# Performance work log

Hardware: AMD Instinct MI355X
Metric: run time of the kernel (lower is better)

The kernel has to match this reference:

```python
import jax, jax.numpy as jnp
import numpy as np

B, NL, C, H, W = 4, 2048, 128, 128, 128
N_PTS0, N_PTS1 = 32, 8
SCALE = N_PTS0 // N_PTS1  # MaxPool1d kernel/stride
FEATURE_DIM = 5
BN_EPS = 1e-5


def setup_inputs() -> dict:
    key = jax.random.key(0)
    ks = jax.random.split(key, 12)
    fm = jax.random.normal(ks[0], (B, C, H, W), dtype=jnp.float32)
    lines = jax.random.uniform(ks[1], (B, NL, 2, 2), dtype=jnp.float32) * 128.0
    P = C // 2
    s = 0.05
    return {
        "feature_map": fm,
        "lines": lines,
        # Bottleneck1D params (BatchNorm in eval mode: running_mean=0, running_var=1)
        "bn1_g": jnp.ones((C,), jnp.float32), "bn1_b": jnp.zeros((C,), jnp.float32),
        "conv1_w": jax.random.normal(ks[2], (P, C, 1), jnp.float32) * s,
        "conv1_b": jnp.zeros((P,), jnp.float32),
        "bn2_g": jnp.ones((P,), jnp.float32), "bn2_b": jnp.zeros((P,), jnp.float32),
        "conv2_w": jax.random.normal(ks[3], (P, P, 3), jnp.float32) * s,
        "conv2_b": jnp.zeros((P,), jnp.float32),
        "bn3_g": jnp.ones((P,), jnp.float32), "bn3_b": jnp.zeros((P,), jnp.float32),
        "conv3_w": jax.random.normal(ks[4], (C, P, 1), jnp.float32) * s,
        "conv3_b": jnp.zeros((C,), jnp.float32),
        # fc2: ReLU -> Linear(dim_loi*n_pts1 + 5, 4)
        "fc2_w": jax.random.normal(ks[5], (4, C * N_PTS1 + FEATURE_DIM), jnp.float32) * s,
        "fc2_b": jnp.zeros((4,), jnp.float32),
    }


def _bn(x, g, b):
    # eval-mode BatchNorm1d with running_mean=0, running_var=1
    return x * (g / jnp.sqrt(1.0 + BN_EPS))[None, :, None] + b[None, :, None]


def _conv1d(x, w, b, pad):
    y = jax.lax.conv_general_dilated(x, w, (1,), [(pad, pad)],
                                     dimension_numbers=("NCH", "OIH", "NCH"))
    return y + b[None, :, None]


def _loi_gather(fm, lines):
    # sample points along each line: [B, NL, N_PTS0, 2]
    lam = jnp.linspace(0.0, 1.0, N_PTS0, dtype=jnp.float32)[None, None, :, None]
    p = lines[:, :, 0:1, :] * lam + lines[:, :, 1:2, :] * (1.0 - lam) - 0.5
    p = p.reshape(B, -1, 2)                      # [B, NL*N_PTS0, 2]
    px, py = p[..., 0], p[..., 1]
    px0 = jnp.clip(jnp.floor(px), 0.0, 127.0)
    py0 = jnp.clip(jnp.floor(py), 0.0, 127.0)
    px1 = jnp.clip(px0 + 1.0, 0.0, 127.0)
    py1 = jnp.clip(py0 + 1.0, 0.0, 127.0)
    px0l, py0l = px0.astype(jnp.int32), py0.astype(jnp.int32)
    px1l, py1l = px1.astype(jnp.int32), py1.astype(jnp.int32)

    gather = jax.vmap(lambda f, yi, xi: f[:, yi, xi])  # [C, P] per image
    # weights exactly as in the torch source
    xp = (gather(fm, py0l, px0l) * ((px1 - px) * (py1 - py))[:, None, :]
          + gather(fm, py1l, px0l) * ((px - px0) * (py1 - py))[:, None, :]
          + gather(fm, py0l, px1l) * ((px1 - px) * (py - py0))[:, None, :]
          + gather(fm, py1l, px1l) * ((px - px0) * (py - py0))[:, None, :])
    # [B, C, NL*N_PTS0] -> [B*NL, C, N_PTS0]
    xp = xp.reshape(B, C, NL, N_PTS0).transpose(0, 2, 1, 3).reshape(B * NL, C, N_PTS0)
    return xp


def reference(feature_map, lines, bn1_g, bn1_b, conv1_w, conv1_b,
              bn2_g, bn2_b, conv2_w, conv2_b, bn3_g, bn3_b,
              conv3_w, conv3_b, fc2_w, fc2_b):
    xp = _loi_gather(feature_map, lines)               # [B*NL, C, N_PTS0]
    # MaxPool1d(SCALE, SCALE)
    x = xp.reshape(B * NL, C, N_PTS1, SCALE).max(axis=-1)
    # Bottleneck1D residual block
    y = jax.nn.relu(_bn(x, bn1_g, bn1_b))
    y = _conv1d(y, conv1_w, conv1_b, 0)
    y = jax.nn.relu(_bn(y, bn2_g, bn2_b))
    y = _conv1d(y, conv2_w, conv2_b, 1)
    y = jax.nn.relu(_bn(y, bn3_g, bn3_b))
    y = _conv1d(y, conv3_w, conv3_b, 0)
    x = x + y                                          # [B*NL, C, N_PTS1]
    # line geometry feature (use_cood=1, use_slop=1)
    xyu, xyv = lines[:, :, 0, :], lines[:, :, 1, :]
    u2v = jnp.sqrt(((xyu - xyv) ** 2).sum(-1, keepdims=True)).clip(min=1e-6)
    f = jnp.concatenate([xyu / 128.0, xyv / 128.0, u2v], axis=-1)
    f = f.reshape(B * NL, FEATURE_DIM)
    # concat + fc2 (ReLU -> Linear)
    x = jnp.concatenate([x.reshape(B * NL, C * N_PTS1), f], axis=1)
    logits = jax.nn.relu(x) @ fc2_w.T + fc2_b
    prob = jax.nn.softmax(logits, axis=1)
    return logits, prob
```

## Files before the change

### kernel.cpp

```cpp
#include <hip/hip_runtime.h>
#include <math.h>

#define BB 4
#define NLL 2048
#define CC 128
#define HH 128
#define WW 128
#define NPTS0 32
#define NPTS1 8
#define PP 64
#define FDIM 5
#define FCK (CC*NPTS1 + FDIM)
#define FCKP 1032

typedef __attribute__((ext_vector_type(8))) short bf16x8;
typedef __attribute__((ext_vector_type(4))) float f32x4;

__device__ __forceinline__ unsigned short f2bf(float f) {
    union { float f; unsigned u; } v; v.f = f;
    unsigned u = v.u;
    return (unsigned short)((u + 0x7fffu + ((u >> 16) & 1u)) >> 16);
}
__device__ __forceinline__ float bf2f(unsigned short s) {
    union { unsigned u; float f; } v; v.u = ((unsigned)s) << 16;
    return v.f;
}

__global__ __launch_bounds__(256)
void transpose_prep(const float* __restrict__ fm, const float* __restrict__ w1,
                    const float* __restrict__ w2, const float* __restrict__ w3,
                    const float* __restrict__ fcw,
                    unsigned short* __restrict__ fmT,
                    unsigned short* __restrict__ W1b,
                    unsigned short* __restrict__ W2b,
                    unsigned short* __restrict__ W3b,
                    float* __restrict__ fcwP) {
    const int t = threadIdx.x;
    if (blockIdx.x >= 512) {
        int gid = (blockIdx.x - 512) * 256 + t;
        for (int e = gid; e < 32800; e += 4096) {
            if (e < 8192) {
                W1b[e] = f2bf(w1[e]);
            } else if (e < 20480) {
                int g = e - 8192;
                int tt = g >> 12, r = g & 4095;
                int p = r >> 6, q = r & 63;
                W2b[tt * 4096 + p * 64 + q] = f2bf(w2[p * 192 + q * 3 + tt]);
            } else if (e < 28672) {
                int g = e - 20480;
                W3b[g] = f2bf(w3[g]);
            } else {
                int g = e - 28672;
                int o = g / FCKP, r = g - o * FCKP;
                fcwP[g] = (r < FCK) ? fcw[o * FCK + r] : 0.0f;
            }
        }
        return;
    }
    __shared__ unsigned short tile[2][128 * 72];
    const int by = blockIdx.x;
    const int b = by >> 7, y = by & 127;
    const float* src = fm + ((size_t)b * CC) * (HH * WW) + (size_t)y * WW;
    const int x4 = (t & 31) * 4;
    const int xh = x4 >> 6, xl = x4 & 63;
    #pragma unroll
    for (int i = 0; i < 16; ++i) {
        int r = (t >> 5) + 8 * i;
        float4 v = *(const float4*)&src[(size_t)r * (HH * WW) + x4];
        ushort4 u;
        u.x = f2bf(v.x); u.y = f2bf(v.y); u.z = f2bf(v.z); u.w = f2bf(v.w);
        *(ushort4*)&tile[xh][r * 72 + (xl ^ (r & 28))] = u;
    }
    __syncthreads();
    const int c4 = (t & 31) * 4;
    #pragma unroll
    for (int h = 0; h < 2; ++h) {
        unsigned short* dst = fmT + ((size_t)by * WW + h * 64) * CC;
        #pragma unroll
        for (int i = 0; i < 8; ++i) {
            int x = (t >> 5) + 8 * i;
            ushort4 u;
            u.x = tile[h][(c4 + 0) * 72 + (x ^ ((c4 + 0) & 28))];
            u.y = tile[h][(c4 + 1) * 72 + (x ^ ((c4 + 1) & 28))];
            u.z = tile[h][(c4 + 2) * 72 + (x ^ ((c4 + 2) & 28))];
            u.w = tile[h][(c4 + 3) * 72 + (x ^ ((c4 + 3) & 28))];
            *(ushort4*)&dst[(size_t)x * CC + c4] = u;
        }
    }
}

__global__ __launch_bounds__(256, 8)
void line_mfma(const unsigned short* __restrict__ fmT,
               const float* __restrict__ lines,
               const float* __restrict__ bn1_g, const float* __restrict__ bn1_b,
               const unsigned short* __restrict__ W1b, const float* __restrict__ b1,
               const float* __restrict__ bn2_g, const float* __restrict__ bn2_b,
               const unsigned short* __restrict__ W2b, const float* __restrict__ b2,
               const float* __restrict__ bn3_g, const float* __restrict__ bn3_b,
               const unsigned short* __restrict__ W3b, const float* __restrict__ b3,
               const float* __restrict__ fcwP,  const float* __restrict__ fcb,
               float* __restrict__ out) {
    __shared__ __align__(16) char smem[19200];
    int*   s_oA = (int*)(smem + 0);
    int*   s_oB = (int*)(smem + 512);
    int*   s_oC = (int*)(smem + 1024);
    int*   s_oD = (int*)(smem + 1536);
    float* s_wA = (float*)(smem + 2048);
    float* s_wB = (float*)(smem + 2560);
    float* s_wC = (float*)(smem + 3072);
    float* s_wD = (float*)(smem + 3584);
    unsigned short* s_z1 = (unsigned short*)(smem + 0);
    unsigned short* s_xs = (unsigned short*)(smem + 5760);
    unsigned short* s_z2 = (unsigned short*)(smem + 14464);
    float* s_red = (float*)(smem + 19072);

    const int bx  = blockIdx.x;
    const int L0  = bx * 4;
    const int b   = bx >> 9;
    const int tid = threadIdx.x;
    const int lane = tid & 63;
    const int wv   = tid >> 6;
    const int quad = lane >> 4;
    const int l16  = lane & 15;
    const float inv_s = 1.0f / sqrtf(1.0f + 1e-5f);

    if (tid < 128) {
        int line = tid >> 5, pt = tid & 31;
        const float* ln = lines + (size_t)(L0 + line) * 4;
        float lam = (float)pt * (1.0f / 31.0f);
        float om  = 1.0f - lam;
        float px = ln[0] * lam + ln[2] * om - 0.5f;
        float py = ln[1] * lam + ln[3] * om - 0.5f;
        float px0 = fminf(fmaxf(floorf(px), 0.0f), 127.0f);
        float py0 = fminf(fmaxf(floorf(py), 0.0f), 127.0f);
        float px1 = fminf(px0 + 1.0f, 127.0f);
        float py1 = fminf(py0 + 1.0f, 127.0f);
        int ix0 = (int)px0, ix1 = (int)px1, iy0 = (int)py0, iy1 = (int)py1;
        s_oA[tid] = (iy0 * WW + ix0) * CC;
        s_oB[tid] = (iy1 * WW + ix0) * CC;
        s_oC[tid] = (iy0 * WW + ix1) * CC;
        s_oD[tid] = (iy1 * WW + ix1) * CC;
        float ax = px1 - px, bxv = px - px0, ay = py1 - py, byv = py - py0;
        s_wA[tid] = ax  * ay;
        s_wB[tid] = bxv * ay;
        s_wC[tid] = ax  * byv;
        s_wD[tid] = bxv * byv;
    }
    __syncthreads();

    #pragma unroll 1
    for (int h = 0; h < 2; ++h) {
        int m = h * 16 + (tid >> 4);
        int line = m >> 3, k = m & 7;
        int c8 = (tid & 15) * 8;
        const unsigned short* base = fmT + (size_t)b * (HH * WW * CC) + c8;
        float acc[8];
        #pragma unroll
        for (int i = 0; i < 8; ++i) acc[i] = -INFINITY;
        #pragma unroll
        for (int j = 0; j < 4; ++j) {
            int pt = line * 32 + k * 4 + j;
            bf16x8 rA = *(const bf16x8*)(base + s_oA[pt]);
            bf16x8 rB = *(const bf16x8*)(base + s_oB[pt]);
            bf16x8 rC = *(const bf16x8*)(base + s_oC[pt]);
            bf16x8 rD = *(const bf16x8*)(base + s_oD[pt]);
            float wA = s_wA[pt], wB = s_wB[pt], wC = s_wC[pt], wD = s_wD[pt];
            #pragma unroll
            for (int i = 0; i < 8; ++i) {
                float v = wA * bf2f((unsigned short)rA[i])
                        + wB * bf2f((unsigned short)rB[i])
                        + wC * bf2f((unsigned short)rC[i])
                        + wD * bf2f((unsigned short)rD[i]);
                acc[i] = fmaxf(acc[i], v);
            }
        }
        bf16x8 pk;
        #pragma unroll
        for (int i = 0; i < 8; ++i) pk[i] = (short)f2bf(acc[i]);
        *(bf16x8*)&s_xs[m * 136 + c8] = pk;
    }
    __syncthreads();

    {
        int mh = wv & 1, nh = wv >> 1;
        int mrow = mh * 16 + l16;
        bf16x8 afr[4];
        #pragma unroll
        for (int kc = 0; kc < 4; ++kc) {
            bf16x8 x = *(const bf16x8*)&s_xs[mrow * 136 + kc * 32 + quad * 8];
            int c0 = kc * 32 + quad * 8;
            float4 g0 = *(const float4*)(bn1_g + c0);
            float4 g1 = *(const float4*)(bn1_g + c0 + 4);
            float4 bb0 = *(const float4*)(bn1_b + c0);
            float4 bb1 = *(const float4*)(bn1_b + c0 + 4);
            float gs[8] = {g0.x, g0.y, g0.z, g0.w, g1.x, g1.y, g1.z, g1.w};
            float bs[8] = {bb0.x, bb0.y, bb0.z, bb0.w, bb1.x, bb1.y, bb1.z, bb1.w};
            bf16x8 pk;
            #pragma unroll
            for (int i = 0; i < 8; ++i) {
                float v = fmaxf(bf2f((unsigned short)x[i]) * (gs[i] * inv_s) + bs[i], 0.0f);
                pk[i] = (short)f2bf(v);
            }
            afr[kc] = pk;
        }
        #pragma unroll
        for (int sub = 0; sub < 2; ++sub) {
            int p = nh * 32 + sub * 16 + l16;
            f32x4 acc = {0.f, 0.f, 0.f, 0.f};
            #pragma unroll
            for (int kc = 0; kc < 4; ++kc) {
                bf16x8 bf = *(const bf16x8*)(W1b + p * 128 + kc * 32 + quad * 8);
                acc = __builtin_amdgcn_mfma_f32_16x16x32_bf16(afr[kc], bf, acc, 0, 0, 0);
            }
            float s2 = bn2_g[p] * inv_s, bb2 = bn2_b[p], cb = b1[p];
            #pragma unroll
            for (int r = 0; r < 4; ++r) {
                int mm = mh * 16 + quad * 4 + r;
                int lline = mm >> 3, kk = mm & 7;
                float v = fmaxf((acc[r] + cb) * s2 + bb2, 0.0f);
                s_z1[lline * 720 + (kk + 1) * 72 + p] = f2bf(v);
            }
        }
        #pragma unroll
        for (int e = tid; e < 512; e += 256) {
            int lline = e >> 7;
            int rr = (e >> 6) & 1;
            int q = e & 63;
            s_z1[lline * 720 + (rr ? 9 : 0) * 72 + q] = 0;
        }
    }
    __syncthreads();

    {
        int mh = wv & 1, nh = wv >> 1;
        int mrow = mh * 16 + l16;
        int linea = mrow >> 3, ka = mrow & 7;
        const unsigned short* arow = s_z1 + linea * 720 + ka * 72;
        bf16x8 afr[3][2];
        #pragma unroll
        for (int t = 0; t < 3; ++t)
            #pragma unroll
            for (int kc = 0; kc < 2; ++kc)
                afr[t][kc] = *(const bf16x8*)&arow[t * 72 + kc * 32 + quad * 8];
        #pragma unroll
        for (int sub = 0; sub < 2; ++sub) {
            int p = nh * 32 + sub * 16 + l16;
            f32x4 acc = {0.f, 0.f, 0.f, 0.f};
            #pragma unroll
            for (int t = 0; t < 3; ++t) {
                #pragma unroll
                for (int kc = 0; kc < 2; ++kc) {
                    bf16x8 bf = *(const bf16x8*)(W2b + t * 4096 + p * 64 + kc * 32 + quad * 8);
                    acc = __builtin_amdgcn_mfma_f32_16x16x32_bf16(afr[t][kc], bf, acc, 0, 0, 0);
                }
            }
            float s3 = bn3_g[p] * inv_s, bb3 = bn3_b[p], cb = b2[p];
            #pragma unroll
            for (int r = 0; r < 4; ++r) {
                int mm = mh * 16 + quad * 4 + r;
                float v = fmaxf((acc[r] + cb) * s3 + bb3, 0.0f);
                s_z2[mm * 72 + p] = f2bf(v);
            }
        }
    }
    __syncthreads();

    float p0 = 0.f, p1 = 0.f, p2 = 0.f, p3 = 0.f;
    {
        int mh = wv & 1;
        int n0 = (wv >> 1) * 64;
        int mrow = mh * 16 + l16;
        bf16x8 a0 = *(const bf16x8*)&s_z2[mrow * 72 + quad * 8];
        bf16x8 a1 = *(const bf16x8*)&s_z2[mrow * 72 + 32 + quad * 8];
        int kbase = (quad & 1) * 4;
        #pragma unroll
        for (int sub = 0; sub < 4; ++sub) {
            int c = n0 + sub * 16 + l16;
            f32x4 acc = {0.f, 0.f, 0.f, 0.f};
            bf16x8 bf0 = *(const bf16x8*)(W3b + c * 64 + quad * 8);
            bf16x8 bf1 = *(const bf16x8*)(W3b + c * 64 + 32 + quad * 8);
            acc = __builtin_amdgcn_mfma_f32_16x16x32_bf16(a0, bf0, acc, 0, 0, 0);
            acc = __builtin_amdgcn_mfma_f32_16x16x32_bf16(a1, bf1, acc, 0, 0, 0);
            float cb = b3[c];
            int idx = c * 8 + kbase;
            float4 w0 = *(const float4*)(fcwP + 0 * FCKP + idx);
            float4 w1v = *(const float4*)(fcwP + 1 * FCKP + idx);
            float4 w2v = *(const float4*)(fcwP + 2 * FCKP + idx);
            float4 w3v = *(const float4*)(fcwP + 3 * FCKP + idx);
            const float* w0a = (const float*)&w0;
            const float* w1a = (const float*)&w1v;
            const float* w2a = (const float*)&w2v;
            const float* w3a = (const float*)&w3v;
            #pragma unroll
            for (int r = 0; r < 4; ++r) {
                int mm = mh * 16 + quad * 4 + r;
                float xv = bf2f(s_xs[mm * 136 + c]);
                float v = fmaxf(xv + acc[r] + cb, 0.0f);
                p0 = fmaf(v, w0a[r], p0);
                p1 = fmaf(v, w1a[r], p1);
                p2 = fmaf(v, w2a[r], p2);
                p3 = fmaf(v, w3a[r], p3);
            }
        }
    }
    #pragma unroll
    for (int off = 16; off >= 1; off >>= 1) {
        p0 += __shfl_down(p0, off);
        p1 += __shfl_down(p1, off);
        p2 += __shfl_down(p2, off);
        p3 += __shfl_down(p3, off);
    }
    if ((lane & 31) == 0) {
        int h = lane >> 5;
        s_red[wv * 8 + h * 4 + 0] = p0;
        s_red[wv * 8 + h * 4 + 1] = p1;
        s_red[wv * 8 + h * 4 + 2] = p2;
        s_red[wv * 8 + h * 4 + 3] = p3;
    }
    __syncthreads();

    if (tid < 4) {
        int line = tid;
        int wa = line >> 1;
        int h  = (line & 1) * 4;
        float lg[4];
        #pragma unroll
        for (int o = 0; o < 4; ++o)
            lg[o] = fcb[o] + s_red[wa * 8 + h + o] + s_red[(wa + 2) * 8 + h + o];
        const float* ln = lines + (size_t)(L0 + line) * 4;
        float ux = ln[0], uy = ln[1], vx = ln[2], vy = ln[3];
        float dx = ux - vx, dy = uy - vy;
        float d = fmaxf(sqrtf(dx * dx + dy * dy), 1e-6f);
        float ft[FDIM] = {ux * (1.0f / 128.0f), uy * (1.0f / 128.0f),
                          vx * (1.0f / 128.0f), vy * (1.0f / 128.0f), d};
        #pragma unroll
        for (int j = 0; j < FDIM; ++j) {
            float fv = fmaxf(ft[j], 0.0f);
            #pragma unroll
            for (int o = 0; o < 4; ++o)
                lg[o] = fmaf(fv, fcwP[o * FCKP + 1024 + j], lg[o]);
        }
        float m = fmaxf(fmaxf(lg[0], lg[1]), fmaxf(lg[2], lg[3]));
        float e0 = expf(lg[0] - m), e1 = expf(lg[1] - m);
        float e2 = expf(lg[2] - m), e3 = expf(lg[3] - m);
        float inv = 1.0f / (e0 + e1 + e2 + e3);
        float* lo = out + (size_t)(L0 + line) * 4;
        lo[0] = lg[0]; lo[1] = lg[1]; lo[2] = lg[2]; lo[3] = lg[3];
        float* pr = out + (size_t)BB * NLL * 4 + (size_t)(L0 + line) * 4;
        pr[0] = e0 * inv; pr[1] = e1 * inv; pr[2] = e2 * inv; pr[3] = e3 * inv;
    }
}

__global__ __launch_bounds__(256)
void transpose_fm2(const float* __restrict__ fm, float* __restrict__ fmT) {
    __shared__ float tile[32 * 132];
    const int c0 = blockIdx.x * 32;
    const int by = blockIdx.y;
    const int b = by >> 7, y = by & 127;
    const int t = threadIdx.x;
    const float* src = fm + ((size_t)b * CC) * (HH * WW) + (size_t)y * WW;
    const int x4 = (t & 31) * 4;
    #pragma unroll
    for (int i = 0; i < 4; ++i) {
        int r = (t >> 5) + 8 * i;
        *(float4*)&tile[r * 132 + x4] =
            *(const float4*)&src[(size_t)(c0 + r) * (HH * WW) + x4];
    }
    __syncthreads();
    float* dst = fmT + (size_t)by * WW * CC + c0 + (t & 31);
    const int cr = (t & 31) * 132;
    #pragma unroll
    for (int i = 0; i < 16; ++i) {
        int x = (t >> 5) + 8 * i;
        dst[(size_t)x * CC] = tile[cr + x];
    }
}

template<bool TRANS>
__global__ __launch_bounds__(256)
void line_kernel_v1(const float* __restrict__ fm,
                    const float* __restrict__ lines,
                    const float* __restrict__ bn1_g, const float* __restrict__ bn1_b,
                    const float* __restrict__ w1,    const float* __restrict__ b1,
                    const float* __restrict__ bn2_g, const float* __restrict__ bn2_b,
                    const float* __restrict__ w2,    const float* __restrict__ b2,
                    const float* __restrict__ bn3_g, const float* __restrict__ bn3_b,
                    const float* __restrict__ w3,    const float* __restrict__ b3,
                    const float* __restrict__ fcw,   const float* __restrict__ fcb,
                    float* __restrict__ out) {
    __shared__ int   s_ix0[32], s_ix1[32], s_iy0[32], s_iy1[32];
    __shared__ float s_wA[32], s_wB[32], s_wC[32], s_wD[32];
    __shared__ float xs [8][132];
    __shared__ float ybn[8][132];
    __shared__ float z1 [64][12];
    __shared__ float z2 [64][8];
    __shared__ float s_feat[8];
    __shared__ float s_red[16];

    const int L   = blockIdx.x;
    const int b   = L / NLL;
    const int tid = threadIdx.x;
    const float inv_s = 1.0f / sqrtf(1.0f + 1e-5f);
    const float* ln = lines + (size_t)L * 4;

    if (tid < 32) {
        float lam = (float)tid * (1.0f / 31.0f);
        float om  = 1.0f - lam;
        float px = ln[0] * lam + ln[2] * om - 0.5f;
        float py = ln[1] * lam + ln[3] * om - 0.5f;
        float px0 = fminf(fmaxf(floorf(px), 0.0f), 127.0f);
        float py0 = fminf(fmaxf(floorf(py), 0.0f), 127.0f);
        float px1 = fminf(px0 + 1.0f, 127.0f);
        float py1 = fminf(py0 + 1.0f, 127.0f);
        s_ix0[tid] = (int)px0; s_ix1[tid] = (int)px1;
        s_iy0[tid] = (int)py0; s_iy1[tid] = (int)py1;
        float ax = px1 - px, bxv = px - px0, ay = py1 - py, byv = py - py0;
        s_wA[tid] = ax  * ay;  s_wB[tid] = bxv * ay;
        s_wC[tid] = ax  * byv; s_wD[tid] = bxv * byv;
    }
    if (tid == 0) {
        float ux = ln[0], uy = ln[1], vx = ln[2], vy = ln[3];
        float dx = ux - vx, dy = uy - vy;
        float d = fmaxf(sqrtf(dx * dx + dy * dy), 1e-6f);
        s_feat[0] = ux / 128.0f; s_feat[1] = uy / 128.0f;
        s_feat[2] = vx / 128.0f; s_feat[3] = vy / 128.0f;
        s_feat[4] = d;
    }
    __syncthreads();
    {
        int cq = tid & 31, k = tid >> 5, c0 = cq * 4;
        float4 acc;
        acc.x = -INFINITY; acc.y = -INFINITY; acc.z = -INFINITY; acc.w = -INFINITY;
        #pragma unroll
        for (int j = 0; j < 4; ++j) {
            int pt = k * 4 + j;
            int ix0 = s_ix0[pt], ix1 = s_ix1[pt];
            int iy0 = s_iy0[pt], iy1 = s_iy1[pt];
            float wA = s_wA[pt], wB = s_wB[pt], wC = s_wC[pt], wD = s_wD[pt];
            float4 vA, vB, vC, vD;
            if (TRANS) {
                const float* base = fm + (size_t)b * HH * WW * CC;
                vA = *(const float4*)(base + ((size_t)(iy0 * WW + ix0)) * CC + c0);
                vB = *(const float4*)(base + ((size_t)(iy1 * WW + ix0)) * CC + c0);
                vC = *(const float4*)(base + ((size_t)(iy0 * WW + ix1)) * CC + c0);
                vD = *(const float4*)(base + ((size_t)(iy1 * WW + ix1)) * CC + c0);
            } else {
                const float* base = fm + ((size_t)b * CC + c0) * HH * WW;
                int oA = iy0 * WW + ix0, oB = iy1 * WW + ix0;
                int oC = iy0 * WW + ix1, oD = iy1 * WW + ix1;
                vA.x = base[oA];           vB.x = base[oB];
                vC.x = base[oC];           vD.x = base[oD];
                vA.y = base[HH*WW + oA];   vB.y = base[HH*WW + oB];
                vC.y = base[HH*WW + oC];   vD.y = base[HH*WW + oD];
                vA.z = base[2*HH*WW + oA]; vB.z = base[2*HH*WW + oB];
                vC.z = base[2*HH*WW + oC]; vD.z = base[2*HH*WW + oD];
                vA.w = base[3*HH*WW + oA]; vB.w = base[3*HH*WW + oB];
                vC.w = base[3*HH*WW + oC]; vD.w = base[3*HH*WW + oD];
            }
            float4 v;
            v.x = wA * vA.x + wB * vB.x + wC * vC.x + wD * vD.x;
            v.y = wA * vA.y + wB * vB.y + wC * vC.y + wD * vD.y;
            v.z = wA * vA.z + wB * vB.z + wC * vC.z + wD * vD.z;
            v.w = wA * vA.w + wB * vB.w + wC * vC.w + wD * vD.w;
            acc.x = fmaxf(acc.x, v.x); acc.y = fmaxf(acc.y, v.y);
            acc.z = fmaxf(acc.z, v.z); acc.w = fmaxf(acc.w, v.w);
        }
        *(float4*)(&xs[k][c0]) = acc;
    }
    __syncthreads();
    for (int e = tid; e < 1024; e += 256) {
        int k = e >> 7, c = e & 127;
        ybn[k][c] = fmaxf(xs[k][c] * (bn1_g[c] * inv_s) + bn1_b[c], 0.0f);
    }
    __syncthreads();
    if (tid < 64) { z1[tid][0] = 0.0f; z1[tid][9] = 0.0f; }
    {
        int p = tid >> 2, kq = tid & 3;
        const float* wrow = w1 + p * 128;
        float a0a = 0.f, a0b = 0.f, a1a = 0.f, a1b = 0.f;
        #pragma unroll 8
        for (int c = 0; c < 128; c += 4) {
            float4 w  = *(const float4*)(wrow + c);
            float4 ya = *(const float4*)(&ybn[kq][c]);
            float4 yb = *(const float4*)(&ybn[kq + 4][c]);
            a0a = fmaf(w.x, ya.x, a0a); a0b = fmaf(w.y, ya.y, a0b);
            a0a = fmaf(w.z, ya.z, a0a); a0b = fmaf(w.w, ya.w, a0b);
            a1a = fmaf(w.x, yb.x, a1a); a1b = fmaf(w.y, yb.y, a1b);
            a1a = fmaf(w.z, yb.z, a1a); a1b = fmaf(w.w, yb.w, a1b);
        }
        float s2 = bn2_g[p] * inv_s, bb = bn2_b[p], cb = b1[p];
        z1[p][1 + kq]     = fmaxf((a0a + a0b + cb) * s2 + bb, 0.0f);
        z1[p][1 + kq + 4] = fmaxf((a1a + a1b + cb) * s2 + bb, 0.0f);
    }
    __syncthreads();
    {
        int p = tid >> 2, kq = tid & 3;
        const float* wrow = w2 + p * 192;
        float acc0 = 0.f, acc1 = 0.f;
        #pragma unroll 4
        for (int q = 0; q < 64; ++q) {
            float w0 = wrow[q * 3 + 0], w1v = wrow[q * 3 + 1], w2v = wrow[q * 3 + 2];
            const float* zr = &z1[q][0];
            acc0 = fmaf(w0, zr[kq], acc0);
            acc0 = fmaf(w1v, zr[kq + 1], acc0);
            acc0 = fmaf(w2v, zr[kq + 2], acc0);
            acc1 = fmaf(w0, zr[kq + 4], acc1);
            acc1 = fmaf(w1v, zr[kq + 5], acc1);
            acc1 = fmaf(w2v, zr[kq + 6], acc1);
        }
        float s3 = bn3_g[p] * inv_s, bb = bn3_b[p], cb = b2[p];
        z2[p][kq]     = fmaxf((acc0 + cb) * s3 + bb, 0.0f);
        z2[p][kq + 4] = fmaxf((acc1 + cb) * s3 + bb, 0.0f);
    }
    __syncthreads();
    float part0 = 0.f, part1 = 0.f, part2 = 0.f, part3 = 0.f;
    {
        int c = tid >> 1, kq = tid & 1;
        const float* wrow = w3 + c * 64;
        float acc[4] = {0.f, 0.f, 0.f, 0.f};
        #pragma unroll 8
        for (int q = 0; q < 64; ++q) {
            float w = wrow[q];
            acc[0] = fmaf(w, z2[q][kq], acc[0]);
            acc[1] = fmaf(w, z2[q][kq + 2], acc[1]);
            acc[2] = fmaf(w, z2[q][kq + 4], acc[2]);
            acc[3] = fmaf(w, z2[q][kq + 6], acc[3]);
        }
        float cb = b3[c];
        #pragma unroll
        for (int i = 0; i < 4; ++i) {
            int k = kq + 2 * i;
            float v = fmaxf(xs[k][c] + acc[i] + cb, 0.0f);
            int idx = c * 8 + k;
            part0 = fmaf(v, fcw[0 * FCK + idx], part0);
            part1 = fmaf(v, fcw[1 * FCK + idx], part1);
            part2 = fmaf(v, fcw[2 * FCK + idx], part2);
            part3 = fmaf(v, fcw[3 * FCK + idx], part3);
        }
    }
    #pragma unroll
    for (int off = 32; off > 0; off >>= 1) {
        part0 += __shfl_down(part0, off);
        part1 += __shfl_down(part1, off);
        part2 += __shfl_down(part2, off);
        part3 += __shfl_down(part3, off);
    }
    if ((tid & 63) == 0) {
        int w = tid >> 6;
        s_red[w * 4 + 0] = part0; s_red[w * 4 + 1] = part1;
        s_red[w * 4 + 2] = part2; s_red[w * 4 + 3] = part3;
    }
    __syncthreads();
    if (tid == 0) {
        float lg[4];
        #pragma unroll
        for (int o = 0; o < 4; ++o)
            lg[o] = fcb[o] + s_red[o] + s_red[4 + o] + s_red[8 + o] + s_red[12 + o];
        #pragma unroll
        for (int j = 0; j < FDIM; ++j) {
            float fv = fmaxf(s_feat[j], 0.0f);
            #pragma unroll
            for (int o = 0; o < 4; ++o)
                lg[o] = fmaf(fv, fcw[o * FCK + 1024 + j], lg[o]);
        }
        float m = fmaxf(fmaxf(lg[0], lg[1]), fmaxf(lg[2], lg[3]));
        float e0 = expf(lg[0] - m), e1 = expf(lg[1] - m);
        float e2 = expf(lg[2] - m), e3 = expf(lg[3] - m);
        float inv = 1.0f / (e0 + e1 + e2 + e3);
        float* lo = out + (size_t)L * 4;
        lo[0] = lg[0]; lo[1] = lg[1]; lo[2] = lg[2]; lo[3] = lg[3];
        float* pr = out + (size_t)BB * NLL * 4 + (size_t)L * 4;
        pr[0] = e0 * inv; pr[1] = e1 * inv; pr[2] = e2 * inv; pr[3] = e3 * inv;
    }
}

extern "C" void kernel_launch(void* const* d_in, const int* in_sizes, int n_in,
                              void* d_out, int out_size, void* d_ws, size_t ws_size,
                              hipStream_t stream) {
    const float* fm     = (const float*)d_in[0];
    const float* lines  = (const float*)d_in[1];
    const float* bn1_g  = (const float*)d_in[2];
    const float* bn1_b  = (const float*)d_in[3];
    const float* w1     = (const float*)d_in[4];
    const float* b1     = (const float*)d_in[5];
    const float* bn2_g  = (const float*)d_in[6];
    const float* bn2_b  = (const float*)d_in[7];
    const float* w2     = (const float*)d_in[8];
    const float* b2     = (const float*)d_in[9];
    const float* bn3_g  = (const float*)d_in[10];
    const float* bn3_b  = (const float*)d_in[11];
    const float* w3     = (const float*)d_in[12];
    const float* b3     = (const float*)d_in[13];
    const float* fcw    = (const float*)d_in[14];
    const float* fcb    = (const float*)d_in[15];
    float* out = (float*)d_out;

    const size_t fmTb_bytes = (size_t)BB * HH * WW * CC * sizeof(unsigned short);
    const size_t fmTf_bytes = (size_t)BB * HH * WW * CC * sizeof(float);
    const size_t wb_bytes   = 57344;
    const size_t fcwP_bytes = 4 * FCKP * sizeof(float);

    if (ws_size >= fmTb_bytes + wb_bytes + fcwP_bytes) {
        unsigned short* fmT = (unsigned short*)d_ws;
        unsigned short* W1b = (unsigned short*)((char*)d_ws + fmTb_bytes);
        unsigned short* W2b = W1b + 8192;
        unsigned short* W3b = W2b + 12288;
        float* fcwP = (float*)((char*)d_ws + fmTb_bytes + wb_bytes);
        transpose_prep<<<512 + 16, 256, 0, stream>>>(
            fm, w1, w2, w3, fcw, fmT, W1b, W2b, W3b, fcwP);
        line_mfma<<<BB * NLL / 4, 256, 0, stream>>>(
            fmT, lines, bn1_g, bn1_b, W1b, b1, bn2_g, bn2_b, W2b, b2,
            bn3_g, bn3_b, W3b, b3, fcwP, fcb, out);
    } else if (ws_size >= fmTf_bytes) {
        float* fmT = (float*)d_ws;
        dim3 tg(CC / 32, BB * HH);
        transpose_fm2<<<tg, 256, 0, stream>>>(fm, fmT);
        line_kernel_v1<true><<<BB * NLL, 256, 0, stream>>>(
            fmT, lines, bn1_g, bn1_b, w1, b1, bn2_g, bn2_b, w2, b2,
            bn3_g, bn3_b, w3, b3, fcw, fcb, out);
    } else {
        line_kernel_v1<false><<<BB * NLL, 256, 0, stream>>>(
            fm, lines, bn1_g, bn1_b, w1, b1, bn2_g, bn2_b, w2, b2,
            bn3_g, bn3_b, w3, b3, fcw, fcb, out);
    }
}
```

Before: 163.6 us.

## Give each wavefront its own two lines to drop block-wide barriers

Restructures line_mfma so that each of the four wavefronts independently processes two lines, each with a private shared-memory region. This removes every __syncthreads and the cross-wave reduction through shared memory. Each block now handles 8 lines instead of 4, which halves the grid and lowers the launch-bounds occupancy hint from 8 to 4. Each wave also issues all 16 gather loads per channel group up front for more memory-level parallelism, at the cost of more registers, more shared memory per block and fewer resident blocks.

```diff
diff --git a/kernel.cpp b/kernel.cpp
--- a/kernel.cpp
+++ b/kernel.cpp
@@ -89,7 +89,7 @@
     }
 }
 
-__global__ __launch_bounds__(256, 8)
+__global__ __launch_bounds__(256, 4)
 void line_mfma(const unsigned short* __restrict__ fmT,
                const float* __restrict__ lines,
                const float* __restrict__ bn1_g, const float* __restrict__ bn1_b,
@@ -100,23 +100,11 @@
                const unsigned short* __restrict__ W3b, const float* __restrict__ b3,
                const float* __restrict__ fcwP,  const float* __restrict__ fcb,
                float* __restrict__ out) {
-    __shared__ __align__(16) char smem[19200];
-    int*   s_oA = (int*)(smem + 0);
-    int*   s_oB = (int*)(smem + 512);
-    int*   s_oC = (int*)(smem + 1024);
-    int*   s_oD = (int*)(smem + 1536);
-    float* s_wA = (float*)(smem + 2048);
-    float* s_wB = (float*)(smem + 2560);
-    float* s_wC = (float*)(smem + 3072);
-    float* s_wD = (float*)(smem + 3584);
-    unsigned short* s_z1 = (unsigned short*)(smem + 0);
-    unsigned short* s_xs = (unsigned short*)(smem + 5760);
-    unsigned short* s_z2 = (unsigned short*)(smem + 14464);
-    float* s_red = (float*)(smem + 19072);
+    __shared__ __align__(16) char smem[4][9536];
 
     const int bx  = blockIdx.x;
-    const int L0  = bx * 4;
-    const int b   = bx >> 9;
+    const int L0  = bx * 8;
+    const int b   = bx >> 8;
     const int tid = threadIdx.x;
     const int lane = tid & 63;
     const int wv   = tid >> 6;
@@ -124,9 +112,16 @@
     const int l16  = lane & 15;
     const float inv_s = 1.0f / sqrtf(1.0f + 1e-5f);
 
-    if (tid < 128) {
-        int line = tid >> 5, pt = tid & 31;
-        const float* ln = lines + (size_t)(L0 + line) * 4;
+    char* wb = smem[wv];
+    unsigned short* s_xs = (unsigned short*)(wb);
+    unsigned short* s_z1 = (unsigned short*)(wb + 4352);
+    unsigned short* s_z2 = (unsigned short*)(wb + 7232);
+    int*   cO = (int*)(wb + 4352);
+    float* cW = (float*)(wb + 4352 + 1024);
+
+    {
+        int line = lane >> 5, pt = lane & 31;
+        const float* ln = lines + (size_t)(L0 + wv * 2 + line) * 4;
         float lam = (float)pt * (1.0f / 31.0f);
         float om  = 1.0f - lam;
         float px = ln[0] * lam + ln[2] * om - 0.5f;
@@ -136,58 +131,67 @@
         float px1 = fminf(px0 + 1.0f, 127.0f);
         float py1 = fminf(py0 + 1.0f, 127.0f);
         int ix0 = (int)px0, ix1 = (int)px1, iy0 = (int)py0, iy1 = (int)py1;
-        s_oA[tid] = (iy0 * WW + ix0) * CC;
-        s_oB[tid] = (iy1 * WW + ix0) * CC;
-        s_oC[tid] = (iy0 * WW + ix1) * CC;
-        s_oD[tid] = (iy1 * WW + ix1) * CC;
+        cO[lane]       = (iy0 * WW + ix0) * CC;
+        cO[64 + lane]  = (iy1 * WW + ix0) * CC;
+        cO[128 + lane] = (iy0 * WW + ix1) * CC;
+        cO[192 + lane] = (iy1 * WW + ix1) * CC;
         float ax = px1 - px, bxv = px - px0, ay = py1 - py, byv = py - py0;
-        s_wA[tid] = ax  * ay;
-        s_wB[tid] = bxv * ay;
-        s_wC[tid] = ax  * byv;
-        s_wD[tid] = bxv * byv;
-    }
-    __syncthreads();
-
-    #pragma unroll 1
-    for (int h = 0; h < 2; ++h) {
-        int m = h * 16 + (tid >> 4);
+        cW[lane]       = ax  * ay;
+        cW[64 + lane]  = bxv * ay;
+        cW[128 + lane] = ax  * byv;
+        cW[192 + lane] = bxv * byv;
+    }
+
+    {
+        int m = lane >> 2;
         int line = m >> 3, k = m & 7;
-        int c8 = (tid & 15) * 8;
-        const unsigned short* base = fmT + (size_t)b * (HH * WW * CC) + c8;
-        float acc[8];
-        #pragma unroll
-        for (int i = 0; i < 8; ++i) acc[i] = -INFINITY;
-        #pragma unroll
-        for (int j = 0; j < 4; ++j) {
-            int pt = line * 32 + k * 4 + j;
-            bf16x8 rA = *(const bf16x8*)(base + s_oA[pt]);
-            bf16x8 rB = *(const bf16x8*)(base + s_oB[pt]);
-            bf16x8 rC = *(const bf16x8*)(base + s_oC[pt]);
-            bf16x8 rD = *(const bf16x8*)(base + s_oD[pt]);
-            float wA = s_wA[pt], wB = s_wB[pt], wC = s_wC[pt], wD = s_wD[pt];
-            #pragma unroll
-            for (int i = 0; i < 8; ++i) {
-                float v = wA * bf2f((unsigned short)rA[i])
-                        + wB * bf2f((unsigned short)rB[i])
-                        + wC * bf2f((unsigned short)rC[i])
-                        + wD * bf2f((unsigned short)rD[i]);
-                acc[i] = fmaxf(acc[i], v);
-            }
-        }
-        bf16x8 pk;
-        #pragma unroll
-        for (int i = 0; i < 8; ++i) pk[i] = (short)f2bf(acc[i]);
-        *(bf16x8*)&s_xs[m * 136 + c8] = pk;
-    }
-    __syncthreads();
-
-    {
-        int mh = wv & 1, nh = wv >> 1;
-        int mrow = mh * 16 + l16;
+        int csb = (lane & 3) * 8;
+        int pi0 = line * 32 + k * 4;
+        const unsigned short* base = fmT + (size_t)b * (HH * WW * CC);
+        #pragma unroll 1
+        for (int cg = 0; cg < 4; ++cg) {
+            int c8 = cg * 32 + csb;
+            const unsigned short* bc = base + c8;
+            bf16x8 rA[4], rB[4], rC[4], rD[4];
+            #pragma unroll
+            for (int j = 0; j < 4; ++j) {
+                rA[j] = *(const bf16x8*)(bc + cO[pi0 + j]);
+                rB[j] = *(const bf16x8*)(bc + cO[64 + pi0 + j]);
+                rC[j] = *(const bf16x8*)(bc + cO[128 + pi0 + j]);
+                rD[j] = *(const bf16x8*)(bc + cO[192 + pi0 + j]);
+            }
+            float acc[8];
+            #pragma unroll
+            for (int i = 0; i < 8; ++i) acc[i] = -INFINITY;
+            #pragma unroll
+            for (int j = 0; j < 4; ++j) {
+                float wA = cW[pi0 + j], wB = cW[64 + pi0 + j];
+                float wC = cW[128 + pi0 + j], wD = cW[192 + pi0 + j];
+                #pragma unroll
+                for (int i = 0; i < 8; ++i) {
+                    float v = wA * bf2f((unsigned short)rA[j][i])
+                            + wB * bf2f((unsigned short)rB[j][i])
+                            + wC * bf2f((unsigned short)rC[j][i])
+                            + wD * bf2f((unsigned short)rD[j][i]);
+                    acc[i] = fmaxf(acc[i], v);
+                }
+            }
+            bf16x8 pk;
+            #pragma unroll
+            for (int i = 0; i < 8; ++i) pk[i] = (short)f2bf(acc[i]);
+            *(bf16x8*)&s_xs[m * 136 + c8] = pk;
+        }
+    }
+
+    {
+        s_z1[0 * 720 + 0 * 72 + lane] = 0;
+        s_z1[0 * 720 + 9 * 72 + lane] = 0;
+        s_z1[1 * 720 + 0 * 72 + lane] = 0;
+        s_z1[1 * 720 + 9 * 72 + lane] = 0;
         bf16x8 afr[4];
         #pragma unroll
         for (int kc = 0; kc < 4; ++kc) {
-            bf16x8 x = *(const bf16x8*)&s_xs[mrow * 136 + kc * 32 + quad * 8];
+            bf16x8 x = *(const bf16x8*)&s_xs[l16 * 136 + kc * 32 + quad * 8];
             int c0 = kc * 32 + quad * 8;
             float4 g0 = *(const float4*)(bn1_g + c0);
             float4 g1 = *(const float4*)(bn1_g + c0 + 4);
@@ -204,8 +208,8 @@
             afr[kc] = pk;
         }
         #pragma unroll
-        for (int sub = 0; sub < 2; ++sub) {
-            int p = nh * 32 + sub * 16 + l16;
+        for (int sub = 0; sub < 4; ++sub) {
+            int p = sub * 16 + l16;
             f32x4 acc = {0.f, 0.f, 0.f, 0.f};
             #pragma unroll
             for (int kc = 0; kc < 4; ++kc) {
@@ -215,26 +219,16 @@
             float s2 = bn2_g[p] * inv_s, bb2 = bn2_b[p], cb = b1[p];
             #pragma unroll
             for (int r = 0; r < 4; ++r) {
-                int mm = mh * 16 + quad * 4 + r;
+                int mm = quad * 4 + r;
                 int lline = mm >> 3, kk = mm & 7;
                 float v = fmaxf((acc[r] + cb) * s2 + bb2, 0.0f);
                 s_z1[lline * 720 + (kk + 1) * 72 + p] = f2bf(v);
             }
         }
-        #pragma unroll
-        for (int e = tid; e < 512; e += 256) {
-            int lline = e >> 7;
-            int rr = (e >> 6) & 1;
-            int q = e & 63;
-            s_z1[lline * 720 + (rr ? 9 : 0) * 72 + q] = 0;
-        }
-    }
-    __syncthreads();
-
-    {
-        int mh = wv & 1, nh = wv >> 1;
-        int mrow = mh * 16 + l16;
-        int linea = mrow >> 3, ka = mrow & 7;
+    }
+
+    {
+        int linea = l16 >> 3, ka = l16 & 7;
         const unsigned short* arow = s_z1 + linea * 720 + ka * 72;
         bf16x8 afr[3][2];
         #pragma unroll
@@ -243,8 +237,8 @@
             for (int kc = 0; kc < 2; ++kc)
                 afr[t][kc] = *(const bf16x8*)&arow[t * 72 + kc * 32 + quad * 8];
         #pragma unroll
-        for (int sub = 0; sub < 2; ++sub) {
-            int p = nh * 32 + sub * 16 + l16;
+        for (int sub = 0; sub < 4; ++sub) {
+            int p = sub * 16 + l16;
             f32x4 acc = {0.f, 0.f, 0.f, 0.f};
             #pragma unroll
             for (int t = 0; t < 3; ++t) {
@@ -257,28 +251,23 @@
             float s3 = bn3_g[p] * inv_s, bb3 = bn3_b[p], cb = b2[p];
             #pragma unroll
             for (int r = 0; r < 4; ++r) {
-                int mm = mh * 16 + quad * 4 + r;
                 float v = fmaxf((acc[r] + cb) * s3 + bb3, 0.0f);
-                s_z2[mm * 72 + p] = f2bf(v);
-            }
-        }
-    }
-    __syncthreads();
+                s_z2[(quad * 4 + r) * 72 + p] = f2bf(v);
+            }
+        }
+    }
 
     float p0 = 0.f, p1 = 0.f, p2 = 0.f, p3 = 0.f;
     {
-        int mh = wv & 1;
-        int n0 = (wv >> 1) * 64;
-        int mrow = mh * 16 + l16;
-        bf16x8 a0 = *(const bf16x8*)&s_z2[mrow * 72 + quad * 8];
-        bf16x8 a1 = *(const bf16x8*)&s_z2[mrow * 72 + 32 + quad * 8];
         int kbase = (quad & 1) * 4;
-        #pragma unroll
-        for (int sub = 0; sub < 4; ++sub) {
-            int c = n0 + sub * 16 + l16;
+        bf16x8 a0 = *(const bf16x8*)&s_z2[l16 * 72 + 0 * 32 + quad * 8];
+        bf16x8 a1 = *(const bf16x8*)&s_z2[l16 * 72 + 1 * 32 + quad * 8];
+        #pragma unroll
+        for (int sub = 0; sub < 8; ++sub) {
+            int c = sub * 16 + l16;
             f32x4 acc = {0.f, 0.f, 0.f, 0.f};
-            bf16x8 bf0 = *(const bf16x8*)(W3b + c * 64 + quad * 8);
-            bf16x8 bf1 = *(const bf16x8*)(W3b + c * 64 + 32 + quad * 8);
+            bf16x8 bf0 = *(const bf16x8*)(W3b + c * 64 + 0 * 32 + quad * 8);
+            bf16x8 bf1 = *(const bf16x8*)(W3b + c * 64 + 1 * 32 + quad * 8);
             acc = __builtin_amdgcn_mfma_f32_16x16x32_bf16(a0, bf0, acc, 0, 0, 0);
             acc = __builtin_amdgcn_mfma_f32_16x16x32_bf16(a1, bf1, acc, 0, 0, 0);
             float cb = b3[c];
@@ -293,7 +282,7 @@
             const float* w3a = (const float*)&w3v;
             #pragma unroll
             for (int r = 0; r < 4; ++r) {
-                int mm = mh * 16 + quad * 4 + r;
+                int mm = quad * 4 + r;
                 float xv = bf2f(s_xs[mm * 136 + c]);
                 float v = fmaxf(xv + acc[r] + cb, 0.0f);
                 p0 = fmaf(v, w0a[r], p0);
@@ -311,23 +300,10 @@
         p3 += __shfl_down(p3, off);
     }
     if ((lane & 31) == 0) {
-        int h = lane >> 5;
-        s_red[wv * 8 + h * 4 + 0] = p0;
-        s_red[wv * 8 + h * 4 + 1] = p1;
-        s_red[wv * 8 + h * 4 + 2] = p2;
-        s_red[wv * 8 + h * 4 + 3] = p3;
-    }
-    __syncthreads();
-
-    if (tid < 4) {
-        int line = tid;
-        int wa = line >> 1;
-        int h  = (line & 1) * 4;
-        float lg[4];
-        #pragma unroll
-        for (int o = 0; o < 4; ++o)
-            lg[o] = fcb[o] + s_red[wa * 8 + h + o] + s_red[(wa + 2) * 8 + h + o];
-        const float* ln = lines + (size_t)(L0 + line) * 4;
+        int line = lane >> 5;
+        int gl = L0 + wv * 2 + line;
+        float lg[4] = {fcb[0] + p0, fcb[1] + p1, fcb[2] + p2, fcb[3] + p3};
+        const float* ln = lines + (size_t)gl * 4;
         float ux = ln[0], uy = ln[1], vx = ln[2], vy = ln[3];
         float dx = ux - vx, dy = uy - vy;
         float d = fmaxf(sqrtf(dx * dx + dy * dy), 1e-6f);
@@ -344,10 +320,10 @@
         float e0 = expf(lg[0] - m), e1 = expf(lg[1] - m);
         float e2 = expf(lg[2] - m), e3 = expf(lg[3] - m);
         float inv = 1.0f / (e0 + e1 + e2 + e3);
-        float* lo = out + (size_t)(L0 + line) * 4;
-        lo[0] = lg[0]; lo[1] = lg[1]; lo[2] = lg[2]; lo[3] = lg[3];
-        float* pr = out + (size_t)BB * NLL * 4 + (size_t)(L0 + line) * 4;
-        pr[0] = e0 * inv; pr[1] = e1 * inv; pr[2] = e2 * inv; pr[3] = e3 * inv;
+        float4 lo = {lg[0], lg[1], lg[2], lg[3]};
+        float4 pr = {e0 * inv, e1 * inv, e2 * inv, e3 * inv};
+        *(float4*)(out + (size_t)gl * 4) = lo;
+        *(float4*)(out + (size_t)BB * NLL * 4 + (size_t)gl * 4) = pr;
     }
 }
 
@@ -608,7 +584,7 @@
         float* fcwP = (float*)((char*)d_ws + fmTb_bytes + wb_bytes);
         transpose_prep<<<512 + 16, 256, 0, stream>>>(
             fm, w1, w2, w3, fcw, fmT, W1b, W2b, W3b, fcwP);
-        line_mfma<<<BB * NLL / 4, 256, 0, stream>>>(
+        line_mfma<<<BB * NLL / 8, 256, 0, stream>>>(
             fmT, lines, bn1_g, bn1_b, W1b, b1, bn2_g, bn2_b, W2b, b2,
             bn3_g, bn3_b, W3b, b3, fcwP, fcb, out);
     } else if (ws_size >= fmTf_bytes) {
```

After: 158.0 us. -3.4%, faster.
